# Kernel optimization log

Hardware: AMD Instinct MI355X
Metric: run time of the kernel (lower is better)

Reference implementation:

```python
import jax, jax.numpy as jnp
import numpy as np

B, C, L, M, F, N = 4, 32, 256, 256, 8, 64  # N = L // 4 per build()


def setup_inputs() -> dict:
    key = jax.random.key(0)
    k1, k2, k3, k4 = jax.random.split(key, 4)
    return {
        "x_real": jax.random.normal(k1, (B, 1, C, L, M), dtype=jnp.float32),
        "x_imag": jax.random.normal(k2, (B, 1, C, L, M), dtype=jnp.float32),
        "w_real": jax.random.normal(k3, (F, C, N, 1), dtype=jnp.float32),
        "w_imag": jax.random.normal(k4, (F, C, N, 1), dtype=jnp.float32),
    }


def _interp_weights(w, L):
    """tfp.math.interp_regular_1d_grid along axis=-2: map x_targ=0..L-1 over
    ref range [0, L-1] onto an N-point regular grid, linear interpolation."""
    Nn = w.shape[-2]
    t = jnp.arange(L, dtype=jnp.float32) / (L - 1) * (Nn - 1)  # grid coords
    lo = jnp.clip(jnp.floor(t).astype(jnp.int32), 0, Nn - 2)
    frac = (t - lo.astype(jnp.float32))[:, None]               # (L, 1)
    return w[:, :, lo, :] * (1.0 - frac) + w[:, :, lo + 1, :] * frac  # (F,C,L,1)


def reference(x_real, x_imag, w_real, w_imag):
    Lm = x_real.shape[-2]
    wr = _interp_weights(w_real, Lm)  # (F, C, L, 1)
    wi = _interp_weights(w_imag, Lm)
    # complex multiply: (wr + i*wi) * (xr + i*xi), broadcast (B,1,C,L,M)->(B,F,C,L,M)
    pr = wr * x_real - wi * x_imag
    pi = wr * x_imag + wi * x_real
    scale = jnp.sqrt(1.0 + jnp.arange(Lm, dtype=jnp.float32))[:, None]  # self.l, (L,1)
    yr = jnp.mean(pr, axis=-3) * scale  # (B, F, L, M)
    yi = jnp.mean(pi, axis=-3) * scale
    yr = jax.nn.relu(yr)  # relu=True: relu applied to real part only
    return jnp.stack([yr, yi])  # (2, B, F, L, M) == (real, imag)
```

## Files before the change

### kernel.cpp

```cpp
#include <hip/hip_runtime.h>
#include <math.h>

constexpr int B_ = 4, C_ = 32, L_ = 256, M_ = 256, F_ = 8, N_ = 64;

__global__ __launch_bounds__(128, 2) void sphereconv_kernel(
    const float* __restrict__ xr, const float* __restrict__ xi,
    const float* __restrict__ wr, const float* __restrict__ wi,
    float* __restrict__ out)
{
    __shared__ float  ws[C_ * 16];
    __shared__ float4 red[16 * 64];

    const int b    = blockIdx.x >> 8;
    const int l    = blockIdx.x & (L_ - 1);
    const int tid  = threadIdx.x;
    const int wave = tid >> 6;
    const int lane = tid & 63;

    const float tc = ((float)l / (float)(L_ - 1)) * (float)(N_ - 1);
    int lo = (int)floorf(tc);
    if (lo > N_ - 2) lo = N_ - 2;
    const float frac = tc - (float)lo;

#pragma unroll
    for (int i = tid; i < C_ * 16; i += 128) {
        const int c = i >> 4;
        const int j = i & 15;
        const int f = j & 7;
        const float* w = (j & 8) ? wi : wr;
        const int base = (f * C_ + c) * N_ + lo;
        ws[c * 16 + j] = w[base] * (1.0f - frac) + w[base + 1] * frac;
    }
    __syncthreads();

    const int c0 = wave * 16;
    const size_t strideC4 = (size_t)L_ * M_ / 4;
    const size_t xoff = ((size_t)b * C_ + c0) * L_ * M_ + (size_t)l * M_ + lane * 4;
    const float4* xr4 = (const float4*)(xr + xoff);
    const float4* xi4 = (const float4*)(xi + xoff);

    float4 xv_r[16], xv_i[16];
#pragma unroll
    for (int c = 0; c < 16; ++c) {
        xv_r[c] = xr4[c * strideC4];
        xv_i[c] = xi4[c * strideC4];
    }

    float4 accr[F_], acci[F_];
#pragma unroll
    for (int f = 0; f < F_; ++f) {
        accr[f] = make_float4(0.f, 0.f, 0.f, 0.f);
        acci[f] = make_float4(0.f, 0.f, 0.f, 0.f);
    }

#define CX(f, A, Bv)                                          \
    accr[f].x = fmaf(A, vr.x, fmaf(-(Bv), vi.x, accr[f].x));  \
    accr[f].y = fmaf(A, vr.y, fmaf(-(Bv), vi.y, accr[f].y));  \
    accr[f].z = fmaf(A, vr.z, fmaf(-(Bv), vi.z, accr[f].z));  \
    accr[f].w = fmaf(A, vr.w, fmaf(-(Bv), vi.w, accr[f].w));  \
    acci[f].x = fmaf(A, vi.x, fmaf((Bv), vr.x, acci[f].x));   \
    acci[f].y = fmaf(A, vi.y, fmaf((Bv), vr.y, acci[f].y));   \
    acci[f].z = fmaf(A, vi.z, fmaf((Bv), vr.z, acci[f].z));   \
    acci[f].w = fmaf(A, vi.w, fmaf((Bv), vr.w, acci[f].w));

#pragma unroll
    for (int c = 0; c < 16; ++c) {
        const float4 vr = xv_r[c];
        const float4 vi = xv_i[c];
        const float* wp = &ws[(c0 + c) * 16];
        const float4 a0 = *(const float4*)(wp + 0);
        const float4 a1 = *(const float4*)(wp + 4);
        const float4 b0 = *(const float4*)(wp + 8);
        const float4 b1 = *(const float4*)(wp + 12);
        CX(0, a0.x, b0.x)
        CX(1, a0.y, b0.y)
        CX(2, a0.z, b0.z)
        CX(3, a0.w, b0.w)
        CX(4, a1.x, b1.x)
        CX(5, a1.y, b1.y)
        CX(6, a1.z, b1.z)
        CX(7, a1.w, b1.w)
    }
#undef CX

    if (wave == 1) {
#pragma unroll
        for (int f = 0; f < F_; ++f) {
            red[(f * 2 + 0) * 64 + lane] = accr[f];
            red[(f * 2 + 1) * 64 + lane] = acci[f];
        }
    }
    __syncthreads();
    if (wave == 0) {
        const float scale = sqrtf(1.0f + (float)l) * (1.0f / (float)C_);
        const size_t o0      = (((size_t)b * F_) * L_ + l) * M_ + lane * 4;
        const size_t imagOff = (size_t)B_ * F_ * L_ * M_;
        const size_t fStride = (size_t)L_ * M_;
#pragma unroll
        for (int f = 0; f < F_; ++f) {
            const float4 pr = red[(f * 2 + 0) * 64 + lane];
            const float4 pi = red[(f * 2 + 1) * 64 + lane];
            float4 yr, yi;
            yr.x = fmaxf((accr[f].x + pr.x) * scale, 0.f);
            yr.y = fmaxf((accr[f].y + pr.y) * scale, 0.f);
            yr.z = fmaxf((accr[f].z + pr.z) * scale, 0.f);
            yr.w = fmaxf((accr[f].w + pr.w) * scale, 0.f);
            yi.x = (acci[f].x + pi.x) * scale;
            yi.y = (acci[f].y + pi.y) * scale;
            yi.z = (acci[f].z + pi.z) * scale;
            yi.w = (acci[f].w + pi.w) * scale;
            *(float4*)(out + o0 + (size_t)f * fStride)           = yr;
            *(float4*)(out + o0 + (size_t)f * fStride + imagOff) = yi;
        }
    }
}

extern "C" void kernel_launch(void* const* d_in, const int* in_sizes, int n_in,
                              void* d_out, int out_size, void* d_ws, size_t ws_size,
                              hipStream_t stream) {
    const float* xr = (const float*)d_in[0];
    const float* xi = (const float*)d_in[1];
    const float* wr = (const float*)d_in[2];
    const float* wi = (const float*)d_in[3];
    float* out = (float*)d_out;
    sphereconv_kernel<<<dim3(B_ * L_), dim3(128), 0, stream>>>(xr, xi, wr, wi, out);
}
```

Baseline: 107.9 us.

## Split M across waves with float2 loads and parallelize real/imag epilogue

Doubles the block to 256 threads, with each wave handling half of the channels and half of the M columns using float2 loads, so per-thread register arrays are halved. The cross-wave reduction is restructured so paired waves exchange data: one wave writes the real outputs and the other writes the imaginary outputs, which keeps every wave active in the epilogue. This is meant to raise occupancy and balance the epilogue. The cost is narrower memory accesses and more threads per block.

```diff
diff --git a/kernel.cpp b/kernel.cpp
--- a/kernel.cpp
+++ b/kernel.cpp
@@ -3,19 +3,21 @@
 
 constexpr int B_ = 4, C_ = 32, L_ = 256, M_ = 256, F_ = 8, N_ = 64;
 
-__global__ __launch_bounds__(128, 2) void sphereconv_kernel(
+__global__ __launch_bounds__(256, 4) void sphereconv_kernel(
     const float* __restrict__ xr, const float* __restrict__ xi,
     const float* __restrict__ wr, const float* __restrict__ wi,
     float* __restrict__ out)
 {
     __shared__ float  ws[C_ * 16];
-    __shared__ float4 red[16 * 64];
+    __shared__ float2 red[4 * F_ * 64];
 
-    const int b    = blockIdx.x >> 8;
-    const int l    = blockIdx.x & (L_ - 1);
-    const int tid  = threadIdx.x;
-    const int wave = tid >> 6;
-    const int lane = tid & 63;
+    const int b     = blockIdx.x >> 8;
+    const int l     = blockIdx.x & (L_ - 1);
+    const int tid   = threadIdx.x;
+    const int wave  = tid >> 6;
+    const int lane  = tid & 63;
+    const int chalf = wave & 1;
+    const int mhalf = wave >> 1;
 
     const float tc = ((float)l / (float)(L_ - 1)) * (float)(N_ - 1);
     int lo = (int)floorf(tc);
@@ -23,7 +25,7 @@
     const float frac = tc - (float)lo;
 
 #pragma unroll
-    for (int i = tid; i < C_ * 16; i += 128) {
+    for (int i = tid; i < C_ * 16; i += 256) {
         const int c = i >> 4;
         const int j = i & 15;
         const int f = j & 7;
@@ -33,40 +35,37 @@
     }
     __syncthreads();
 
-    const int c0 = wave * 16;
-    const size_t strideC4 = (size_t)L_ * M_ / 4;
-    const size_t xoff = ((size_t)b * C_ + c0) * L_ * M_ + (size_t)l * M_ + lane * 4;
-    const float4* xr4 = (const float4*)(xr + xoff);
-    const float4* xi4 = (const float4*)(xi + xoff);
+    const int c0 = chalf * 16;
+    const int m  = mhalf * 128 + lane * 2;
+    const size_t strideC2 = (size_t)L_ * M_ / 2;
+    const size_t xoff = ((size_t)b * C_ + c0) * (size_t)L_ * M_ + (size_t)l * M_ + m;
+    const float2* xr2 = (const float2*)(xr + xoff);
+    const float2* xi2 = (const float2*)(xi + xoff);
 
-    float4 xv_r[16], xv_i[16];
+    float2 xv_r[16], xv_i[16];
 #pragma unroll
     for (int c = 0; c < 16; ++c) {
-        xv_r[c] = xr4[c * strideC4];
-        xv_i[c] = xi4[c * strideC4];
+        xv_r[c] = xr2[c * strideC2];
+        xv_i[c] = xi2[c * strideC2];
     }
 
-    float4 accr[F_], acci[F_];
+    float2 accr[F_], acci[F_];
 #pragma unroll
     for (int f = 0; f < F_; ++f) {
-        accr[f] = make_float4(0.f, 0.f, 0.f, 0.f);
-        acci[f] = make_float4(0.f, 0.f, 0.f, 0.f);
+        accr[f] = make_float2(0.f, 0.f);
+        acci[f] = make_float2(0.f, 0.f);
     }
 
 #define CX(f, A, Bv)                                          \
     accr[f].x = fmaf(A, vr.x, fmaf(-(Bv), vi.x, accr[f].x));  \
     accr[f].y = fmaf(A, vr.y, fmaf(-(Bv), vi.y, accr[f].y));  \
-    accr[f].z = fmaf(A, vr.z, fmaf(-(Bv), vi.z, accr[f].z));  \
-    accr[f].w = fmaf(A, vr.w, fmaf(-(Bv), vi.w, accr[f].w));  \
     acci[f].x = fmaf(A, vi.x, fmaf((Bv), vr.x, acci[f].x));   \
-    acci[f].y = fmaf(A, vi.y, fmaf((Bv), vr.y, acci[f].y));   \
-    acci[f].z = fmaf(A, vi.z, fmaf((Bv), vr.z, acci[f].z));   \
-    acci[f].w = fmaf(A, vi.w, fmaf((Bv), vr.w, acci[f].w));
+    acci[f].y = fmaf(A, vi.y, fmaf((Bv), vr.y, acci[f].y));
 
 #pragma unroll
     for (int c = 0; c < 16; ++c) {
-        const float4 vr = xv_r[c];
-        const float4 vi = xv_i[c];
+        const float2 vr = xv_r[c];
+        const float2 vi = xv_i[c];
         const float* wp = &ws[(c0 + c) * 16];
         const float4 a0 = *(const float4*)(wp + 0);
         const float4 a1 = *(const float4*)(wp + 4);
@@ -83,34 +82,37 @@
     }
 #undef CX
 
-    if (wave == 1) {
+    {
+        float2* myexp = &red[wave * F_ * 64];
+#pragma unroll
+        for (int f = 0; f < F_; ++f)
+            myexp[f * 64 + lane] = (wave & 1) ? accr[f] : acci[f];
+    }
+    __syncthreads();
+
+    const float scale = sqrtf(1.0f + (float)l) * (1.0f / (float)C_);
+    const size_t fStride = (size_t)L_ * M_;
+    const size_t o0 = (((size_t)b * F_) * (size_t)L_ + l) * M_ + m;
+    if ((wave & 1) == 0) {
+        const float2* pr = &red[(wave + 1) * F_ * 64];
 #pragma unroll
         for (int f = 0; f < F_; ++f) {
-            red[(f * 2 + 0) * 64 + lane] = accr[f];
-            red[(f * 2 + 1) * 64 + lane] = acci[f];
+            const float2 p = pr[f * 64 + lane];
+            float2 y;
+            y.x = fmaxf((accr[f].x + p.x) * scale, 0.f);
+            y.y = fmaxf((accr[f].y + p.y) * scale, 0.f);
+            *(float2*)(out + o0 + (size_t)f * fStride) = y;
         }
-    }
-    __syncthreads();
-    if (wave == 0) {
-        const float scale = sqrtf(1.0f + (float)l) * (1.0f / (float)C_);
-        const size_t o0      = (((size_t)b * F_) * L_ + l) * M_ + lane * 4;
+    } else {
         const size_t imagOff = (size_t)B_ * F_ * L_ * M_;
-        const size_t fStride = (size_t)L_ * M_;
+        const float2* pi = &red[(wave - 1) * F_ * 64];
 #pragma unroll
         for (int f = 0; f < F_; ++f) {
-            const float4 pr = red[(f * 2 + 0) * 64 + lane];
-            const float4 pi = red[(f * 2 + 1) * 64 + lane];
-            float4 yr, yi;
-            yr.x = fmaxf((accr[f].x + pr.x) * scale, 0.f);
-            yr.y = fmaxf((accr[f].y + pr.y) * scale, 0.f);
-            yr.z = fmaxf((accr[f].z + pr.z) * scale, 0.f);
-            yr.w = fmaxf((accr[f].w + pr.w) * scale, 0.f);
-            yi.x = (acci[f].x + pi.x) * scale;
-            yi.y = (acci[f].y + pi.y) * scale;
-            yi.z = (acci[f].z + pi.z) * scale;
-            yi.w = (acci[f].w + pi.w) * scale;
-            *(float4*)(out + o0 + (size_t)f * fStride)           = yr;
-            *(float4*)(out + o0 + (size_t)f * fStride + imagOff) = yi;
+            const float2 p = pi[f * 64 + lane];
+            float2 y;
+            y.x = (acci[f].x + p.x) * scale;
+            y.y = (acci[f].y + p.y) * scale;
+            *(float2*)(out + o0 + (size_t)f * fStride + imagOff) = y;
         }
     }
 }
@@ -123,5 +125,5 @@
     const float* wr = (const float*)d_in[2];
     const float* wi = (const float*)d_in[3];
     float* out = (float*)d_out;
-    sphereconv_kernel<<<dim3(B_ * L_), dim3(128), 0, stream>>>(xr, xi, wr, wi, out);
+    sphereconv_kernel<<<dim3(B_ * L_), dim3(256), 0, stream>>>(xr, xi, wr, wi, out);
 }
```

Result: faster. 104.6 us (median of 2 runs) (-3.1%).

## Assign one m column per thread over all channels, drop cross-wave reduction

Applied to the files above, without the earlier changes.

The block grows to 256 threads, and each thread now owns a single m element and sums all 32 channels itself. Before, two waves each took half the channels and handled four m values as float4. This removes the shared-memory reduction and its second barrier, and raises occupancy through launch bounds of 256 threads with 4 blocks. Loads and stores become scalar and use nontemporal hints, at the cost of narrower memory transactions and more shared-memory weight reads per unit of output.

```diff
diff --git a/kernel.cpp b/kernel.cpp
--- a/kernel.cpp
+++ b/kernel.cpp
@@ -3,19 +3,19 @@
 
 constexpr int B_ = 4, C_ = 32, L_ = 256, M_ = 256, F_ = 8, N_ = 64;
 
-__global__ __launch_bounds__(128, 2) void sphereconv_kernel(
+__global__ __launch_bounds__(256, 4) void sphereconv_kernel(
     const float* __restrict__ xr, const float* __restrict__ xi,
     const float* __restrict__ wr, const float* __restrict__ wi,
     float* __restrict__ out)
 {
-    __shared__ float  ws[C_ * 16];
-    __shared__ float4 red[16 * 64];
+    __shared__ float ws[C_ * 16];
 
     const int b    = blockIdx.x >> 8;
     const int l    = blockIdx.x & (L_ - 1);
     const int tid  = threadIdx.x;
     const int wave = tid >> 6;
     const int lane = tid & 63;
+    const int m    = wave * 64 + lane;
 
     const float tc = ((float)l / (float)(L_ - 1)) * (float)(N_ - 1);
     int lo = (int)floorf(tc);
@@ -23,51 +23,42 @@
     const float frac = tc - (float)lo;
 
 #pragma unroll
-    for (int i = tid; i < C_ * 16; i += 128) {
+    for (int k = 0; k < 2; ++k) {
+        const int i = tid + k * 256;
         const int c = i >> 4;
         const int j = i & 15;
         const int f = j & 7;
         const float* w = (j & 8) ? wi : wr;
         const int base = (f * C_ + c) * N_ + lo;
-        ws[c * 16 + j] = w[base] * (1.0f - frac) + w[base + 1] * frac;
+        ws[i] = w[base] * (1.0f - frac) + w[base + 1] * frac;
     }
     __syncthreads();
 
-    const int c0 = wave * 16;
-    const size_t strideC4 = (size_t)L_ * M_ / 4;
-    const size_t xoff = ((size_t)b * C_ + c0) * L_ * M_ + (size_t)l * M_ + lane * 4;
-    const float4* xr4 = (const float4*)(xr + xoff);
-    const float4* xi4 = (const float4*)(xi + xoff);
+    const size_t strideC = (size_t)L_ * M_;
+    const size_t xoff = ((size_t)b * C_) * strideC + (size_t)l * M_ + m;
+    const float* xrp = xr + xoff;
+    const float* xip = xi + xoff;
 
-    float4 xv_r[16], xv_i[16];
+    float xvr[C_], xvi[C_];
 #pragma unroll
-    for (int c = 0; c < 16; ++c) {
-        xv_r[c] = xr4[c * strideC4];
-        xv_i[c] = xi4[c * strideC4];
+    for (int c = 0; c < C_; ++c) {
+        xvr[c] = __builtin_nontemporal_load(xrp + (size_t)c * strideC);
+        xvi[c] = __builtin_nontemporal_load(xip + (size_t)c * strideC);
     }
 
-    float4 accr[F_], acci[F_];
+    float accr[F_], acci[F_];
 #pragma unroll
-    for (int f = 0; f < F_; ++f) {
-        accr[f] = make_float4(0.f, 0.f, 0.f, 0.f);
-        acci[f] = make_float4(0.f, 0.f, 0.f, 0.f);
-    }
+    for (int f = 0; f < F_; ++f) { accr[f] = 0.f; acci[f] = 0.f; }
 
-#define CX(f, A, Bv)                                          \
-    accr[f].x = fmaf(A, vr.x, fmaf(-(Bv), vi.x, accr[f].x));  \
-    accr[f].y = fmaf(A, vr.y, fmaf(-(Bv), vi.y, accr[f].y));  \
-    accr[f].z = fmaf(A, vr.z, fmaf(-(Bv), vi.z, accr[f].z));  \
-    accr[f].w = fmaf(A, vr.w, fmaf(-(Bv), vi.w, accr[f].w));  \
-    acci[f].x = fmaf(A, vi.x, fmaf((Bv), vr.x, acci[f].x));   \
-    acci[f].y = fmaf(A, vi.y, fmaf((Bv), vr.y, acci[f].y));   \
-    acci[f].z = fmaf(A, vi.z, fmaf((Bv), vr.z, acci[f].z));   \
-    acci[f].w = fmaf(A, vi.w, fmaf((Bv), vr.w, acci[f].w));
+#define CX(f, A, Bv)                                    \
+    accr[f] = fmaf(A, vr, fmaf(-(Bv), vi, accr[f]));    \
+    acci[f] = fmaf(A, vi, fmaf((Bv), vr, acci[f]));
 
 #pragma unroll
-    for (int c = 0; c < 16; ++c) {
-        const float4 vr = xv_r[c];
-        const float4 vi = xv_i[c];
-        const float* wp = &ws[(c0 + c) * 16];
+    for (int c = 0; c < C_; ++c) {
+        const float vr = xvr[c];
+        const float vi = xvi[c];
+        const float* wp = &ws[c * 16];
         const float4 a0 = *(const float4*)(wp + 0);
         const float4 a1 = *(const float4*)(wp + 4);
         const float4 b0 = *(const float4*)(wp + 8);
@@ -83,35 +74,16 @@
     }
 #undef CX
 
-    if (wave == 1) {
+    const float scale = sqrtf(1.0f + (float)l) * (1.0f / (float)C_);
+    const size_t fStride = strideC;
+    const size_t o0      = (((size_t)b * F_) * (size_t)L_ + l) * M_ + m;
+    const size_t imagOff = (size_t)B_ * F_ * L_ * M_;
 #pragma unroll
-        for (int f = 0; f < F_; ++f) {
-            red[(f * 2 + 0) * 64 + lane] = accr[f];
-            red[(f * 2 + 1) * 64 + lane] = acci[f];
-        }
-    }
-    __syncthreads();
-    if (wave == 0) {
-        const float scale = sqrtf(1.0f + (float)l) * (1.0f / (float)C_);
-        const size_t o0      = (((size_t)b * F_) * L_ + l) * M_ + lane * 4;
-        const size_t imagOff = (size_t)B_ * F_ * L_ * M_;
-        const size_t fStride = (size_t)L_ * M_;
-#pragma unroll
-        for (int f = 0; f < F_; ++f) {
-            const float4 pr = red[(f * 2 + 0) * 64 + lane];
-            const float4 pi = red[(f * 2 + 1) * 64 + lane];
-            float4 yr, yi;
-            yr.x = fmaxf((accr[f].x + pr.x) * scale, 0.f);
-            yr.y = fmaxf((accr[f].y + pr.y) * scale, 0.f);
-            yr.z = fmaxf((accr[f].z + pr.z) * scale, 0.f);
-            yr.w = fmaxf((accr[f].w + pr.w) * scale, 0.f);
-            yi.x = (acci[f].x + pi.x) * scale;
-            yi.y = (acci[f].y + pi.y) * scale;
-            yi.z = (acci[f].z + pi.z) * scale;
-            yi.w = (acci[f].w + pi.w) * scale;
-            *(float4*)(out + o0 + (size_t)f * fStride)           = yr;
-            *(float4*)(out + o0 + (size_t)f * fStride + imagOff) = yi;
-        }
+    for (int f = 0; f < F_; ++f) {
+        const float yr = fmaxf(accr[f] * scale, 0.f);
+        const float yi = acci[f] * scale;
+        __builtin_nontemporal_store(yr, out + o0 + (size_t)f * fStride);
+        __builtin_nontemporal_store(yi, out + o0 + (size_t)f * fStride + imagOff);
     }
 }
 
@@ -123,5 +95,5 @@
     const float* wr = (const float*)d_in[2];
     const float* wi = (const float*)d_in[3];
     float* out = (float*)d_out;
-    sphereconv_kernel<<<dim3(B_ * L_), dim3(128), 0, stream>>>(xr, xi, wr, wi, out);
+    sphereconv_kernel<<<dim3(B_ * L_), dim3(256), 0, stream>>>(xr, xi, wr, wi, out);
 }
```

New measurement: 113.3 us. 5.0% more time.
